# Optimization experiments

Hardware: AMD Instinct MI355X
Metric: run time of the kernel (lower is better)

## Reference

```python
import jax, jax.numpy as jnp
import numpy as np

D, H, L, B = 32, 1024, 2, 4096


def _masks(d, h):
    # Sequential (natural) ordering degrees, as in MADE.create_masks
    d_in = jnp.arange(d)                      # input degrees
    d_hid = jnp.arange(h) % (d - 1)           # hidden degrees
    d_out = jnp.arange(d) % d - 1             # output degrees (= arange(d)-1)
    m0 = (d_hid[:, None] >= d_in[None, :]).astype(jnp.float32)   # [H, D]
    mh = (d_hid[:, None] >= d_hid[None, :]).astype(jnp.float32)  # [H, H]
    mo = (d_out[:, None] >= d_hid[None, :]).astype(jnp.float32)  # [D, H]
    mo = jnp.concatenate([mo, mo], axis=0)                       # [2D, H] (mask.repeat(2,1))
    return m0, mh, mo


def setup_inputs() -> dict:
    key = jax.random.key(0)
    ks = jax.random.split(key, 7)
    u = lambda k, shape, fan_in: jax.random.uniform(
        k, shape, minval=-1.0 / np.sqrt(fan_in), maxval=1.0 / np.sqrt(fan_in), dtype=jnp.float32)
    return {
        "z": jax.random.normal(ks[0], (B, D), dtype=jnp.float32),
        "W0": u(ks[1], (H, D), D),
        "b0": u(ks[2], (H,), D),
        "Wh": u(ks[3], (L, H, H), H),
        "bh": u(ks[4], (L, H), H),
        "Wout": u(ks[5], (2 * D, H), H),
        "bout": u(ks[6], (2 * D,), H),
    }


def reference(z, W0, b0, Wh, bh, Wout, bout):
    d = z.shape[1]
    h = W0.shape[0]
    m0, mh, mo = _masks(d, h)
    MW0 = m0 * W0                 # [H, D]
    MWh = mh[None, :, :] * Wh     # [L, H, H]
    MWo = mo * Wout               # [2D, H]

    def net(x):  # masked MLP: [B, D] -> [B, 2D]
        a = jax.nn.relu(x @ MW0.T + b0)
        for i in range(MWh.shape[0]):  # small fixed layer count
            a = jax.nn.relu(a @ MWh[i].T + bh[i])
        return a @ MWo.T + bout

    def step(x, idx):
        theta = net(x)  # [B, 2D]
        mu = jax.lax.dynamic_slice_in_dim(theta, idx, 1, axis=1)[:, 0]
        log_std = jax.lax.dynamic_slice_in_dim(theta, idx + d, 1, axis=1)[:, 0]
        zi = jax.lax.dynamic_slice_in_dim(z, idx, 1, axis=1)[:, 0]
        xi = zi * jnp.exp(log_std) + mu
        x = jax.lax.dynamic_update_slice(x, xi[:, None], (0, idx))
        return x, None

    x0 = jnp.zeros_like(z)
    x, _ = jax.lax.scan(step, x0, jnp.arange(d, dtype=jnp.int32))
    return x
```

## Files before the change

### kernel.cpp

```cpp
#include <hip/hip_runtime.h>
#include <hip/hip_bf16.h>

#define B_ 4096
#define D_ 32
#define H_ 1024
#define CS 512
#define WPK_L 1079296

typedef __attribute__((ext_vector_type(8))) short short8;
typedef __attribute__((ext_vector_type(4))) float floatx4;

#define BAR() __asm__ __volatile__("s_waitcnt lgkmcnt(0)\n\ts_barrier" ::: "memory")

__device__ inline unsigned short f2bf(float f) {
    unsigned u = __float_as_uint(f);
    unsigned r = (u + 0x7FFF + ((u >> 16) & 1)) >> 16;
    return (unsigned short)r;
}
__device__ inline void glds16(const void* g, void* l) {
    __builtin_amdgcn_global_load_lds(
        (const __attribute__((address_space(1))) unsigned int*)g,
        (__attribute__((address_space(3))) unsigned int*)l, 16, 0, 0);
}

__device__ inline int degs(int hp) { return (hp < 34) ? 0 : (hp - 1) / 33; }
__device__ inline int permf(int hp) {
    int d = degs(hp);
    int r = d ? (hp - 33 * d - 1) : hp;
    return d + 31 * r;
}
__device__ inline int band0i(int idx) {
    int nb0 = (idx == 1) ? 0 : 33 * idx - 32;
    return (nb0 > H_ - 64) ? H_ - 64 : nb0;
}

__global__ __launch_bounds__(256) void prep1(
        const float* __restrict__ Wh, const float* __restrict__ W0,
        const float* __restrict__ Wout, const float* __restrict__ b0,
        const float* __restrict__ bh,
        unsigned short* __restrict__ Wbp, unsigned short* __restrict__ W0pk,
        unsigned short* __restrict__ Wopk, float* __restrict__ b0p,
        float* __restrict__ bhp) {
    __shared__ float row[H_];
    int b = blockIdx.x, t = threadIdx.x;
    if (b < 2048) {
        int l = b >> 10, np = b & 1023;
        const float* src = Wh + ((size_t)l << 20) + ((size_t)permf(np) << 10);
        ((float4*)row)[t] = ((const float4*)src)[t];
        __syncthreads();
        int dn = degs(np);
        unsigned short o[4];
        #pragma unroll
        for (int j = 0; j < 4; j++) {
            int kp = t * 4 + j;
            o[j] = (dn >= degs(kp)) ? f2bf(row[permf(kp)]) : (unsigned short)0;
        }
        ((ushort4*)(Wbp + ((size_t)l << 20) + ((size_t)np << 10)))[t] =
            ushort4{o[0], o[1], o[2], o[3]};
    } else if (b < 2079) {
        int idx = b - 2047;
        int nb0 = band0i(idx);
        int j = t >> 2, ko = (t & 3) * 8;
        int n = nb0 + j;
        int dn = degs(n);
        const float* srow = W0 + (size_t)permf(n) * 32;
        union { unsigned short o[8]; uint4 v; } u;
        #pragma unroll
        for (int e = 0; e < 8; e++)
            u.o[e] = (dn >= ko + e) ? f2bf(srow[ko + e]) : (unsigned short)0;
        *(uint4*)(W0pk + (idx - 1) * 2048 + j * 32 + ko) = u.v;
    } else if (b < 3103) {
        int bb = b - 2079;
        int idx = bb >> 5, c = bb & 31;
        int ns = idx ? 33 * idx + 1 : 0;
        #pragma unroll
        for (int uu = 0; uu < 2; uu++) {
            int e = t + uu * 256;
            int col = e >> 5, k = e & 31;
            int h = c * 32 + k;
            unsigned short v = 0;
            if (col < 2 && h < ns)
                v = f2bf(Wout[(size_t)(idx + col * 32) * H_ + permf(h)]);
            Wopk[(size_t)bb * 512 + e] = v;
        }
    } else {
        int tt = (b - 3103) * 256 + t;
        int hp = tt & 1023;
        int p = permf(hp);
        if (tt < 1024) b0p[hp] = b0[p];
        else if (tt < 2048) bhp[hp] = bh[p];
        else bhp[1024 + hp] = bh[1024 + p];
    }
}

__global__ __launch_bounds__(256) void prep2(const unsigned short* __restrict__ Wbp,
                                             unsigned short* __restrict__ Wpk) {
    int b = blockIdx.x;
    int l = b / 992;
    int r = b - l * 992;
    int idx = (r >> 5) + 1;
    int c = r & 31;
    if (c >= idx + 1) return;
    int nb0 = band0i(idx);
    int t = threadIdx.x;
    int j = t >> 2, ko = (t & 3) * 8;
    uint4 v = *(const uint4*)(Wbp + ((size_t)l << 20) + ((size_t)(nb0 + j) << 10) + c * 32 + ko);
    *(uint4*)(Wpk + (size_t)l * WPK_L + (size_t)1024 * (idx - 1) * (idx + 2)
              + c * 2048 + j * 32 + ko) = v;
}

__device__ inline floatx4 mfma16(short8 a, short8 b, floatx4 c) {
    return __builtin_amdgcn_mfma_f32_16x16x32_bf16(a, b, c, 0, 0, 0);
}

__device__ inline floatx4 band_partial(const unsigned short* act, const unsigned short* wpk,
                                       int frow, int fk, int s, int c0, int c1) {
    const unsigned short* ap = act + frow * 32 + fk * 8;
    const unsigned short* wp = wpk + s * 512 + frow * 32 + fk * 8;
    floatx4 x = {0.f, 0.f, 0.f, 0.f}, y = {0.f, 0.f, 0.f, 0.f};
    int c = c0;
    for (; c + 1 < c1; c += 2) {
        short8 a0 = *(const short8*)(ap + c * CS);
        short8 b0 = *(const short8*)(wp + (size_t)c * 2048);
        short8 a1 = *(const short8*)(ap + (c + 1) * CS);
        short8 b1 = *(const short8*)(wp + (size_t)(c + 1) * 2048);
        x = mfma16(a0, b0, x);
        y = mfma16(a1, b1, y);
    }
    if (c < c1) {
        short8 a0 = *(const short8*)(ap + c * CS);
        short8 b0 = *(const short8*)(wp + (size_t)c * 2048);
        x = mfma16(a0, b0, x);
    }
    return x + y;
}

__global__ __launch_bounds__(1024) void mega_kernel(
        const float* __restrict__ z,
        const unsigned short* __restrict__ W0pk,
        const float* __restrict__ b0p,
        const unsigned short* __restrict__ Wpk,
        const float* __restrict__ bhp,
        const unsigned short* __restrict__ Wopk,
        const float* __restrict__ bout,
        float* __restrict__ xout) {
    __shared__ unsigned short aS[3 * 32 * CS];
    __shared__ unsigned short xbS[16 * 32];
    __shared__ float xsS[512];
    __shared__ float zsS[512];
    __shared__ floatx4 redS[12 * 64];
    __shared__ float redO[16 * 32];
    __shared__ uint4 dummyS[64];

    const int tid = threadIdx.x;
    const int wave = tid >> 6, lane = tid & 63;
    const int frow = lane & 15, fk = lane >> 4;
    const int arow = frow * 32 + fk * 8;
    const int s = wave & 3, q = wave >> 2;
    const int m0 = blockIdx.x * 16;

    {
        uint4 zz = {0u, 0u, 0u, 0u};
        for (int i = tid; i < 3 * 32 * CS / 8; i += 1024) ((uint4*)aS)[i] = zz;
        if (tid < 64)  ((uint4*)xbS)[tid] = zz;
        if (tid < 128) ((uint4*)xsS)[tid] = zz;
        if (tid < 128) ((uint4*)redO)[tid] = zz;
        if (tid < 128) ((float4*)zsS)[tid] = ((const float4*)(z + (size_t)m0 * 32))[tid];
    }
    __syncthreads();

    unsigned short* a1 = aS;
    unsigned short* a2 = aS + 32 * CS;
    unsigned short* a3 = aS + 64 * CS;

    for (int idx = 0; idx < 32; idx++) {
        if (idx > 0) {
            const int nb0 = band0i(idx);
            const int slot = nb0 + s * 16 + frow;
            const int nk = idx + 1;
            const int nk4 = (nk + 3) >> 2;
            const int c0 = q * nk4;
            const int c1m = (c0 + nk4 < nk) ? c0 + nk4 : nk;
            const unsigned short* wb2 = Wpk + (size_t)1024 * (idx - 1) * (idx + 2);
            const unsigned short* wb3 = wb2 + WPK_L;
            const int wsl = (slot >> 5) * CS + (slot & 31);

            if (q == 0) {
                short8 a = *(const short8*)(xbS + frow * 32 + fk * 8);
                short8 bf = *(const short8*)(W0pk + (idx - 1) * 2048 + (s * 16 + frow) * 32 + fk * 8);
                floatx4 acc = {0.f, 0.f, 0.f, 0.f};
                acc = mfma16(a, bf, acc);
                float bb = b0p[slot];
                #pragma unroll
                for (int r = 0; r < 4; r++)
                    a1[wsl + (fk * 4 + r) * 32] = f2bf(fmaxf(acc[r] + bb, 0.f));
            }
            BAR();

            {
                floatx4 p = band_partial(a1, wb2, frow, fk, s, c0, c1m);
                if (q) redS[((q - 1) * 4 + s) * 64 + lane] = p;
                BAR();
                if (q == 0) {
                    p = p + redS[s * 64 + lane] + redS[(4 + s) * 64 + lane]
                          + redS[(8 + s) * 64 + lane];
                    float bb = bhp[slot];
                    #pragma unroll
                    for (int r = 0; r < 4; r++)
                        a2[wsl + (fk * 4 + r) * 32] = f2bf(fmaxf(p[r] + bb, 0.f));
                }
                BAR();
            }

            {
                floatx4 g = band_partial(a2, wb3, frow, fk, s, c0, c1m);
                if (q) redS[((q - 1) * 4 + s) * 64 + lane] = g;
                BAR();
                if (q == 0) {
                    g = g + redS[s * 64 + lane] + redS[(4 + s) * 64 + lane]
                          + redS[(8 + s) * 64 + lane];
                    float bb = bhp[H_ + slot];
                    #pragma unroll
                    for (int r = 0; r < 4; r++)
                        a3[wsl + (fk * 4 + r) * 32] = f2bf(fmaxf(g[r] + bb, 0.f));
                }
                BAR();
            }
        }

        {
            floatx4 oacc = {0.f, 0.f, 0.f, 0.f};
            #pragma unroll
            for (int cc = 0; cc < 2; cc++) {
                int c = wave * 2 + cc;
                short8 a = *(const short8*)(a3 + c * CS + arow);
                short8 bf = *(const short8*)(Wopk + (size_t)((idx * 32 + c) * 16 + frow) * 32 + fk * 8);
                oacc = mfma16(a, bf, oacc);
            }
            if (frow < 2) {
                #pragma unroll
                for (int r = 0; r < 4; r++)
                    redO[wave * 32 + frow * 16 + fk * 4 + r] = oacc[r];
            }
        }

        if (idx < 31) {
            const int slice = (blockIdx.x >> 3) & 31;
            const char* w2n = (const char*)(Wpk + (size_t)1024 * idx * (idx + 3));
            const char* w3n = w2n + (size_t)WPK_L * 2;
            const int bytesn = (idx + 2) * 4096;
            const char* won = (const char*)(Wopk + (size_t)(idx + 1) * 32 * 512);
            int off = (slice & 7) * 16384;
            if (off < bytesn) {
                glds16(w2n + off + tid * 16, dummyS);
                glds16(w3n + off + tid * 16, dummyS);
            }
            glds16(won + (slice & 1) * 16384 + tid * 16, dummyS);
        }
        BAR();

        if (tid < 16) {
            float sm = bout[idx], sl = bout[idx + D_];
            #pragma unroll
            for (int w = 0; w < 16; w++) {
                sm += redO[w * 32 + tid];
                sl += redO[w * 32 + 16 + tid];
            }
            float xi = fmaf(zsS[tid * 32 + idx], expf(sl), sm);
            xsS[tid * 32 + idx] = xi;
            xbS[tid * 32 + idx] = f2bf(xi);
        }
        BAR();
    }

    __syncthreads();
    if (tid < 128)
        ((float4*)(xout + (size_t)m0 * 32))[tid] = ((const float4*)xsS)[tid];
}

extern "C" void kernel_launch(void* const* d_in, const int* in_sizes, int n_in,
                              void* d_out, int out_size, void* d_ws, size_t ws_size,
                              hipStream_t stream) {
    const float* z    = (const float*)d_in[0];
    const float* W0   = (const float*)d_in[1];
    const float* b0   = (const float*)d_in[2];
    const float* Wh   = (const float*)d_in[3];
    const float* bh   = (const float*)d_in[4];
    const float* Wout = (const float*)d_in[5];
    const float* bout = (const float*)d_in[6];

    float* x = (float*)d_out;
    unsigned short* Wbp  = (unsigned short*)d_ws;
    unsigned short* Wpk  = Wbp + 2 * H_ * H_;
    unsigned short* W0pk = Wpk + 2 * WPK_L;
    unsigned short* Wopk = W0pk + 31 * 2048;
    float* b0p = (float*)(Wopk + 32 * 32 * 512);
    float* bhp = b0p + H_;

    prep1<<<3115, 256, 0, stream>>>(Wh, W0, Wout, b0, bh, Wbp, W0pk, Wopk, b0p, bhp);
    prep2<<<2 * 31 * 32, 256, 0, stream>>>(Wbp, Wpk);

    mega_kernel<<<B_ / 16, 1024, 0, stream>>>(z, W0pk, b0p, Wpk, bhp, Wopk, bout, x);
}
```

Before: 220.4 us.

## Restructure per-step schedule: fold new-band output into layer-3 epilogue, prefetch earlier

Realigns the band start to a 32-column boundary. The output projection now runs at the start of each step on the previous a3, using only the older bands, while the newly computed band's contribution to mu/log_std is folded into the layer-3 epilogue through fp32 weights and shuffle reductions. Layer-0 for the next step is moved to wave 0 right after xi is produced, biases and output weights are staged in LDS, and L2 prefetches are issued earlier. The aim is to remove barriers and serial phases per autoregressive step, at the cost of more LDS use and more complex indexing.

```diff
diff --git a/kernel.cpp b/kernel.cpp
--- a/kernel.cpp
+++ b/kernel.cpp
@@ -29,9 +29,9 @@
     int r = d ? (hp - 33 * d - 1) : hp;
     return d + 31 * r;
 }
-__device__ inline int band0i(int idx) {
-    int nb0 = (idx == 1) ? 0 : 33 * idx - 32;
-    return (nb0 > H_ - 64) ? H_ - 64 : nb0;
+__device__ inline int band0a(int idx) {
+    int nb = (33 * (idx - 1) + 1) & ~31;
+    return (nb > H_ - 64) ? H_ - 64 : nb;
 }
 
 __global__ __launch_bounds__(256) void prep1(
@@ -39,8 +39,8 @@
         const float* __restrict__ Wout, const float* __restrict__ b0,
         const float* __restrict__ bh,
         unsigned short* __restrict__ Wbp, unsigned short* __restrict__ W0pk,
-        unsigned short* __restrict__ Wopk, float* __restrict__ b0p,
-        float* __restrict__ bhp) {
+        unsigned short* __restrict__ Wopk, float* __restrict__ Wof32,
+        float* __restrict__ b0p, float* __restrict__ bhp) {
     __shared__ float row[H_];
     int b = blockIdx.x, t = threadIdx.x;
     if (b < 2048) {
@@ -59,7 +59,7 @@
             ushort4{o[0], o[1], o[2], o[3]};
     } else if (b < 2079) {
         int idx = b - 2047;
-        int nb0 = band0i(idx);
+        int nb0 = band0a(idx);
         int j = t >> 2, ko = (t & 3) * 8;
         int n = nb0 + j;
         int dn = degs(n);
@@ -72,19 +72,29 @@
     } else if (b < 3103) {
         int bb = b - 2079;
         int idx = bb >> 5, c = bb & 31;
-        int ns = idx ? 33 * idx + 1 : 0;
+        int limit = idx ? band0a(idx) : 0;
         #pragma unroll
         for (int uu = 0; uu < 2; uu++) {
             int e = t + uu * 256;
             int col = e >> 5, k = e & 31;
             int h = c * 32 + k;
             unsigned short v = 0;
-            if (col < 2 && h < ns)
+            if (col < 2 && h < limit)
                 v = f2bf(Wout[(size_t)(idx + col * 32) * H_ + permf(h)]);
             Wopk[(size_t)bb * 512 + e] = v;
         }
+    } else if (b < 3119) {
+        int e = (b - 3103) * 256 + t;
+        int idx = e >> 7, j = (e >> 1) & 63, c01 = e & 1;
+        float v = 0.f;
+        if (idx >= 1) {
+            int nb = band0a(idx);
+            if (nb + j < 33 * idx + 1)
+                v = Wout[(size_t)(idx + c01 * 32) * H_ + permf(nb + j)];
+        }
+        Wof32[e] = v;
     } else {
-        int tt = (b - 3103) * 256 + t;
+        int tt = (b - 3119) * 256 + t;
         int hp = tt & 1023;
         int p = permf(hp);
         if (tt < 1024) b0p[hp] = b0[p];
@@ -101,7 +111,7 @@
     int idx = (r >> 5) + 1;
     int c = r & 31;
     if (c >= idx + 1) return;
-    int nb0 = band0i(idx);
+    int nb0 = band0a(idx);
     int t = threadIdx.x;
     int j = t >> 2, ko = (t & 3) * 8;
     uint4 v = *(const uint4*)(Wbp + ((size_t)l << 20) + ((size_t)(nb0 + j) << 10) + c * 32 + ko);
@@ -142,14 +152,18 @@
         const unsigned short* __restrict__ Wpk,
         const float* __restrict__ bhp,
         const unsigned short* __restrict__ Wopk,
+        const float* __restrict__ Wof32,
         const float* __restrict__ bout,
         float* __restrict__ xout) {
     __shared__ unsigned short aS[3 * 32 * CS];
-    __shared__ unsigned short xbS[16 * 32];
+    __shared__ unsigned short xbS[512];
     __shared__ float xsS[512];
     __shared__ float zsS[512];
     __shared__ floatx4 redS[12 * 64];
-    __shared__ float redO[16 * 32];
+    __shared__ float redO[2 * 512];
+    __shared__ float redF[128];
+    __shared__ float b0S[1024], bhS[2048], boutS[64];
+    __shared__ float wofS[4096];
     __shared__ uint4 dummyS[64];
 
     const int tid = threadIdx.x;
@@ -164,8 +178,14 @@
         for (int i = tid; i < 3 * 32 * CS / 8; i += 1024) ((uint4*)aS)[i] = zz;
         if (tid < 64)  ((uint4*)xbS)[tid] = zz;
         if (tid < 128) ((uint4*)xsS)[tid] = zz;
-        if (tid < 128) ((uint4*)redO)[tid] = zz;
+        if (tid < 256) ((uint4*)redO)[tid] = zz;
+        if (tid < 32)  ((uint4*)redF)[tid] = zz;
         if (tid < 128) ((float4*)zsS)[tid] = ((const float4*)(z + (size_t)m0 * 32))[tid];
+        b0S[tid] = b0p[tid];
+        bhS[tid] = bhp[tid]; bhS[tid + 1024] = bhp[tid + 1024];
+        if (tid < 64) boutS[tid] = bout[tid];
+        #pragma unroll
+        for (int u = 0; u < 4; u++) wofS[u * 1024 + tid] = Wof32[u * 1024 + tid];
     }
     __syncthreads();
 
@@ -174,8 +194,26 @@
     unsigned short* a3 = aS + 64 * CS;
 
     for (int idx = 0; idx < 32; idx++) {
+        float* rOp = redO + ((idx & 1) << 9);
+
+        {
+            floatx4 oacc = {0.f, 0.f, 0.f, 0.f};
+            #pragma unroll
+            for (int cc = 0; cc < 2; cc++) {
+                int c = wave * 2 + cc;
+                short8 a = *(const short8*)(a3 + c * CS + arow);
+                short8 bf = *(const short8*)(Wopk + (size_t)((idx * 32 + c) * 16 + frow) * 32 + fk * 8);
+                oacc = mfma16(a, bf, oacc);
+            }
+            if (frow < 2) {
+                #pragma unroll
+                for (int r = 0; r < 4; r++)
+                    rOp[wave * 32 + frow * 16 + fk * 4 + r] = oacc[r];
+            }
+        }
+
         if (idx > 0) {
-            const int nb0 = band0i(idx);
+            const int nb0 = band0a(idx);
             const int slot = nb0 + s * 16 + frow;
             const int nk = idx + 1;
             const int nk4 = (nk + 3) >> 2;
@@ -185,16 +223,6 @@
             const unsigned short* wb3 = wb2 + WPK_L;
             const int wsl = (slot >> 5) * CS + (slot & 31);
 
-            if (q == 0) {
-                short8 a = *(const short8*)(xbS + frow * 32 + fk * 8);
-                short8 bf = *(const short8*)(W0pk + (idx - 1) * 2048 + (s * 16 + frow) * 32 + fk * 8);
-                floatx4 acc = {0.f, 0.f, 0.f, 0.f};
-                acc = mfma16(a, bf, acc);
-                float bb = b0p[slot];
-                #pragma unroll
-                for (int r = 0; r < 4; r++)
-                    a1[wsl + (fk * 4 + r) * 32] = f2bf(fmaxf(acc[r] + bb, 0.f));
-            }
             BAR();
 
             {
@@ -204,7 +232,7 @@
                 if (q == 0) {
                     p = p + redS[s * 64 + lane] + redS[(4 + s) * 64 + lane]
                           + redS[(8 + s) * 64 + lane];
-                    float bb = bhp[slot];
+                    float bb = bhS[slot];
                     #pragma unroll
                     for (int r = 0; r < 4; r++)
                         a2[wsl + (fk * 4 + r) * 32] = f2bf(fmaxf(p[r] + bb, 0.f));
@@ -215,62 +243,98 @@
             {
                 floatx4 g = band_partial(a2, wb3, frow, fk, s, c0, c1m);
                 if (q) redS[((q - 1) * 4 + s) * 64 + lane] = g;
+
+                if (idx < 31) {
+                    const int slice = (blockIdx.x >> 3) & 31;
+                    const char* w2n = (const char*)(Wpk + (size_t)1024 * idx * (idx + 3));
+                    const char* w3n = w2n + (size_t)WPK_L * 2;
+                    const int bytesn = (idx + 2) * 4096;
+                    const char* won = (const char*)(Wopk + (size_t)(idx + 1) * 32 * 512);
+                    int off = (slice & 7) * 16384;
+                    if (off < bytesn) {
+                        glds16(w2n + off + tid * 16, dummyS);
+                        glds16(w3n + off + tid * 16, dummyS);
+                    }
+                    glds16(won + (slice & 1) * 16384 + tid * 16, dummyS);
+                    if (tid < 256) glds16((const char*)(W0pk + idx * 2048) + tid * 16, dummyS);
+                }
                 BAR();
                 if (q == 0) {
                     g = g + redS[s * 64 + lane] + redS[(4 + s) * 64 + lane]
                           + redS[(8 + s) * 64 + lane];
-                    float bb = bhp[H_ + slot];
+                    float bb = bhS[1024 + slot];
+                    float v[4];
                     #pragma unroll
-                    for (int r = 0; r < 4; r++)
-                        a3[wsl + (fk * 4 + r) * 32] = f2bf(fmaxf(g[r] + bb, 0.f));
+                    for (int r = 0; r < 4; r++) {
+                        v[r] = fmaxf(g[r] + bb, 0.f);
+                        a3[wsl + (fk * 4 + r) * 32] = f2bf(v[r]);
+                    }
+                    float wmu = wofS[(idx * 64 + s * 16 + frow) * 2 + 0];
+                    float wls = wofS[(idx * 64 + s * 16 + frow) * 2 + 1];
+                    float pm[4], pl[4];
+                    #pragma unroll
+                    for (int r = 0; r < 4; r++) { pm[r] = v[r] * wmu; pl[r] = v[r] * wls; }
+                    #pragma unroll
+                    for (int off = 1; off < 16; off <<= 1) {
+                        #pragma unroll
+                        for (int r = 0; r < 4; r++) {
+                            pm[r] += __shfl_xor(pm[r], off);
+                            pl[r] += __shfl_xor(pl[r], off);
+                        }
+                    }
+                    if (frow == 0) {
+                        #pragma unroll
+                        for (int r = 0; r < 4; r++) {
+                            redF[s * 32 + fk * 4 + r]      = pm[r];
+                            redF[s * 32 + 16 + fk * 4 + r] = pl[r];
+                        }
+                    }
                 }
-                BAR();
-            }
-        }
-
-        {
-            floatx4 oacc = {0.f, 0.f, 0.f, 0.f};
+            }
+        } else {
+            const int slice = (blockIdx.x >> 3) & 31;
+            int off = (slice & 7) * 16384;
+            if (off < 2 * 4096) {
+                glds16((const char*)Wpk + off + tid * 16, dummyS);
+                glds16((const char*)(Wpk + WPK_L) + off + tid * 16, dummyS);
+            }
+            glds16((const char*)(Wopk + (size_t)32 * 512) + (slice & 1) * 16384 + tid * 16, dummyS);
+            if (tid < 256) glds16((const char*)W0pk + tid * 16, dummyS);
+        }
+        BAR();
+
+        if (tid < 16) {
+            float sm = boutS[idx], sl2 = boutS[idx + D_];
             #pragma unroll
-            for (int cc = 0; cc < 2; cc++) {
-                int c = wave * 2 + cc;
-                short8 a = *(const short8*)(a3 + c * CS + arow);
-                short8 bf = *(const short8*)(Wopk + (size_t)((idx * 32 + c) * 16 + frow) * 32 + fk * 8);
-                oacc = mfma16(a, bf, oacc);
-            }
-            if (frow < 2) {
+            for (int w = 0; w < 16; w++) {
+                sm += rOp[w * 32 + tid];
+                sl2 += rOp[w * 32 + 16 + tid];
+            }
+            #pragma unroll
+            for (int t4 = 0; t4 < 4; t4++) {
+                sm += redF[t4 * 32 + tid];
+                sl2 += redF[t4 * 32 + 16 + tid];
+            }
+            float xi = fmaf(zsS[tid * 32 + idx], expf(sl2), sm);
+            xsS[tid * 32 + idx] = xi;
+            xbS[tid * 32 + idx] = f2bf(xi);
+        }
+        if (wave == 0 && idx < 31) {
+            const int nb0n = band0a(idx + 1);
+            short8 xa = *(const short8*)(xbS + frow * 32 + fk * 8);
+            #pragma unroll
+            for (int t4 = 0; t4 < 4; t4++) {
+                short8 wb = *(const short8*)(W0pk + idx * 2048 + (t4 * 16 + frow) * 32 + fk * 8);
+                floatx4 acc = {0.f, 0.f, 0.f, 0.f};
+                acc = mfma16(xa, wb, acc);
+                int sl = nb0n + t4 * 16 + frow;
+                float bb = b0S[sl];
+                int ws2 = (sl >> 5) * CS + (sl & 31);
                 #pragma unroll
                 for (int r = 0; r < 4; r++)
-                    redO[wave * 32 + frow * 16 + fk * 4 + r] = oacc[r];
-            }
-        }
-
-        if (idx < 31) {
-            const int slice = (blockIdx.x >> 3) & 31;
-            const char* w2n = (const char*)(Wpk + (size_t)1024 * idx * (idx + 3));
-            const char* w3n = w2n + (size_t)WPK_L * 2;
-            const int bytesn = (idx + 2) * 4096;
-            const char* won = (const char*)(Wopk + (size_t)(idx + 1) * 32 * 512);
-            int off = (slice & 7) * 16384;
-            if (off < bytesn) {
-                glds16(w2n + off + tid * 16, dummyS);
-                glds16(w3n + off + tid * 16, dummyS);
-            }
-            glds16(won + (slice & 1) * 16384 + tid * 16, dummyS);
-        }
-        BAR();
-
-        if (tid < 16) {
-            float sm = bout[idx], sl = bout[idx + D_];
-            #pragma unroll
-            for (int w = 0; w < 16; w++) {
-                sm += redO[w * 32 + tid];
-                sl += redO[w * 32 + 16 + tid];
-            }
-            float xi = fmaf(zsS[tid * 32 + idx], expf(sl), sm);
-            xsS[tid * 32 + idx] = xi;
-            xbS[tid * 32 + idx] = f2bf(xi);
-        }
-        BAR();
+                    a1[ws2 + (fk * 4 + r) * 32] = f2bf(fmaxf(acc[r] + bb, 0.f));
+            }
+        }
     }
 
     __syncthreads();
@@ -294,11 +358,12 @@
     unsigned short* Wpk  = Wbp + 2 * H_ * H_;
     unsigned short* W0pk = Wpk + 2 * WPK_L;
     unsigned short* Wopk = W0pk + 31 * 2048;
-    float* b0p = (float*)(Wopk + 32 * 32 * 512);
+    float* Wof32 = (float*)(Wopk + 32 * 32 * 512);
+    float* b0p = Wof32 + 4096;
     float* bhp = b0p + H_;
 
-    prep1<<<3115, 256, 0, stream>>>(Wh, W0, Wout, b0, bh, Wbp, W0pk, Wopk, b0p, bhp);
+    prep1<<<3131, 256, 0, stream>>>(Wh, W0, Wout, b0, bh, Wbp, W0pk, Wopk, Wof32, b0p, bhp);
     prep2<<<2 * 31 * 32, 256, 0, stream>>>(Wbp, Wpk);
 
-    mega_kernel<<<B_ / 16, 1024, 0, stream>>>(z, W0pk, b0p, Wpk, bhp, Wopk, bout, x);
-}
+    mega_kernel<<<B_ / 16, 1024, 0, stream>>>(z, W0pk, b0p, Wpk, bhp, Wopk, Wof32, bout, x);
+}
```

Result: no change. 223.6 us (+1.5%).
